# Optimization experiments

Measured on AMD Instinct MI355X. Metric: run time of the kernel, lower is better.

## Reference

```python
import jax, jax.numpy as jnp
import numpy as np

N_NODES = 100000
N_EDGES = 400000
N_GRAPHS = 1000
DIM = 5
N_OUT = 2
EPS = 1e-5


def _linear_params(key, fan_in, fan_out):
    kw, kb = jax.random.split(key)
    s = 1.0 / np.sqrt(fan_in)
    w = jax.random.uniform(kw, (fan_in, fan_out), minval=-s, maxval=s, dtype=jnp.float32)
    b = jax.random.uniform(kb, (fan_out,), minval=-s, maxval=s, dtype=jnp.float32)
    return w, b


def _gn_params(c):
    # rows: [weight, bias, mean_scale] as in PyG GraphNorm init (1, 0, 1)
    return jnp.stack([jnp.ones((c,)), jnp.zeros((c,)), jnp.ones((c,))], axis=0).astype(jnp.float32)


def setup_inputs() -> dict:
    key = jax.random.key(0)
    ks = jax.random.split(key, 16)
    x = jax.random.normal(ks[0], (N_NODES, DIM), dtype=jnp.float32)
    edge_index = jax.random.randint(ks[1], (2, N_EDGES), 0, N_NODES, dtype=jnp.int64)
    batch = jnp.sort(jax.random.randint(ks[2], (N_NODES,), 0, N_GRAPHS, dtype=jnp.int64))
    c1_w1, c1_b1 = _linear_params(ks[3], 2 * DIM, 128)
    c1_w2, c1_b2 = _linear_params(ks[4], 128, 128)
    c1_w3, c1_b3 = _linear_params(ks[5], 128, 128)
    c2_w1, c2_b1 = _linear_params(ks[6], 2 * 128, 256)
    c2_w2, c2_b2 = _linear_params(ks[7], 256, 256)
    c3_w1, c3_b1 = _linear_params(ks[8], 2 * 256, 256)
    lin_w1, lin_b1 = _linear_params(ks[9], 256, 256)
    lin_w2, lin_b2 = _linear_params(ks[10], 256, N_OUT)
    return {
        "x": x, "edge_index": edge_index, "batch": batch,
        "c1_w1": c1_w1, "c1_b1": c1_b1, "c1_gn1": _gn_params(128),
        "c1_w2": c1_w2, "c1_b2": c1_b2, "c1_gn2": _gn_params(128),
        "c1_w3": c1_w3, "c1_b3": c1_b3, "c1_gn3": _gn_params(128),
        "c2_w1": c2_w1, "c2_b1": c2_b1, "c2_gn1": _gn_params(256),
        "c2_w2": c2_w2, "c2_b2": c2_b2, "c2_gn2": _gn_params(256),
        "c3_w1": c3_w1, "c3_b1": c3_b1, "c3_gn1": _gn_params(256),
        "lin_w1": lin_w1, "lin_b1": lin_b1, "lin_w2": lin_w2, "lin_b2": lin_b2,
    }


def _graph_norm(h, p):
    # PyG GraphNorm with batch=None: normalize over all rows (single graph)
    g, b, ms = p[0], p[1], p[2]
    m = h.mean(axis=0)
    out = h - ms * m
    var = (out * out).mean(axis=0)
    return g * out * jax.lax.rsqrt(var + EPS) + b


def _edge_conv(x, src, dst, layers):
    # EdgeConv message: nn(cat[x_i, x_j - x_i]) aggregated (mean) at target i
    xi = x[dst]                                     # [E, C]
    h = jnp.concatenate([xi, x[src] - xi], axis=-1)  # [E, 2C]
    for w, b, gp in layers:
        h = jax.nn.relu(_graph_norm(h @ w + b, gp))
    s = jax.ops.segment_sum(h, dst, num_segments=N_NODES)
    ones = jnp.ones((dst.shape[0], 1), dtype=h.dtype)
    cnt = jax.ops.segment_sum(ones, dst, num_segments=N_NODES)
    return s / jnp.maximum(cnt, 1.0)


def reference(x, edge_index, batch,
              c1_w1, c1_b1, c1_gn1, c1_w2, c1_b2, c1_gn2, c1_w3, c1_b3, c1_gn3,
              c2_w1, c2_b1, c2_gn1, c2_w2, c2_b2, c2_gn2,
              c3_w1, c3_b1, c3_gn1,
              lin_w1, lin_b1, lin_w2, lin_b2):
    src, dst = edge_index[0], edge_index[1]
    h = _edge_conv(x, src, dst, [(c1_w1, c1_b1, c1_gn1), (c1_w2, c1_b2, c1_gn2), (c1_w3, c1_b3, c1_gn3)])
    h = _edge_conv(h, src, dst, [(c2_w1, c2_b1, c2_gn1), (c2_w2, c2_b2, c2_gn2)])
    h = _edge_conv(h, src, dst, [(c3_w1, c3_b1, c3_gn1)])
    # global_mean_pool over graphs (dropout = identity in eval)
    gs = jax.ops.segment_sum(h, batch, num_segments=N_GRAPHS)
    gc = jax.ops.segment_sum(jnp.ones((h.shape[0], 1), h.dtype), batch, num_segments=N_GRAPHS)
    g = gs / jnp.maximum(gc, 1.0)                   # [G, 256]
    out = jax.nn.relu(g @ lin_w1 + lin_b1) @ lin_w2 + lin_b2  # [G, n_out]
    return out
```

## Files before the change

kernel.cpp:

```cpp
#include <hip/hip_runtime.h>
#include <hip/hip_bf16.h>

#define NN 100000
#define NE 400000
#define NG 1000

typedef __attribute__((ext_vector_type(8))) short bf16x8;
typedef __attribute__((ext_vector_type(4))) float f32x4;

__device__ __forceinline__ float bf2f(unsigned short h) {
    return __uint_as_float((unsigned)h << 16);
}
__device__ __forceinline__ unsigned short f2bf(float f) {
    unsigned u = __float_as_uint(f);
    return (unsigned short)((u + 0x7FFFu + ((u >> 16) & 1u)) >> 16);
}
__device__ __forceinline__ void up8(uint4 u, float v[8]) {
    v[0] = bf2f((unsigned short)u.x); v[1] = bf2f((unsigned short)(u.x >> 16));
    v[2] = bf2f((unsigned short)u.y); v[3] = bf2f((unsigned short)(u.y >> 16));
    v[4] = bf2f((unsigned short)u.z); v[5] = bf2f((unsigned short)(u.z >> 16));
    v[6] = bf2f((unsigned short)u.w); v[7] = bf2f((unsigned short)(u.w >> 16));
}
__device__ __forceinline__ uint4 pk8(const float v[8]) {
    uint4 r;
    r.x = (uint)f2bf(v[0]) | ((uint)f2bf(v[1]) << 16);
    r.y = (uint)f2bf(v[2]) | ((uint)f2bf(v[3]) << 16);
    r.z = (uint)f2bf(v[4]) | ((uint)f2bf(v[5]) << 16);
    r.w = (uint)f2bf(v[6]) | ((uint)f2bf(v[7]) << 16);
    return r;
}

__global__ void diag_kernel(float* __restrict__ out, int n, float val) {
    int i = blockIdx.x * 256 + threadIdx.x;
    if (i < n) out[i] = val;
}

__global__ void deg_kernel(const int* __restrict__ dst, int* __restrict__ deg) {
    int e = blockIdx.x * 256 + threadIdx.x;
    if (e < NE) atomicAdd(&deg[dst[e]], 1);
}

__global__ void invdeg_kernel(const int* __restrict__ deg, float* __restrict__ invdeg) {
    int n = blockIdx.x * 256 + threadIdx.x;
    if (n < NN) invdeg[n] = 1.0f / (float)(deg[n] > 0 ? deg[n] : 1);
}

__global__ void conv1_node_kernel(const float* __restrict__ x, const float* __restrict__ W,
                                  unsigned short* __restrict__ RQ) {
    __shared__ float Ws[1280];
    for (int i = threadIdx.x; i < 1280; i += 256) Ws[i] = W[i];
    __syncthreads();
    int c = threadIdx.x & 127;
    int which = threadIdx.x >> 7;
    for (int n = blockIdx.x; n < NN; n += gridDim.x) {
        float acc = 0.f;
        #pragma unroll
        for (int r = 0; r < 5; r++) {
            float xv = x[n * 5 + r];
            float bot = Ws[(5 + r) * 128 + c];
            float w = which ? bot : (Ws[r * 128 + c] - bot);
            acc = fmaf(xv, w, acc);
        }
        RQ[(size_t)n * 256 + threadIdx.x] = f2bf(acc);
    }
}

__global__ void wtrans_kernel(const float* __restrict__ W, unsigned short* __restrict__ Wt,
                              int K, int N) {
    int idx = blockIdx.x * 256 + threadIdx.x;
    if (idx >= K * N) return;
    int c = idx / K, k = idx - c * K;
    Wt[(size_t)c * K + k] = f2bf(W[(size_t)k * N + c]);
}

__global__ void wprime_t_kernel(const float* __restrict__ W, unsigned short* __restrict__ Wpt,
                                int K, int C) {
    int idx = blockIdx.x * 256 + threadIdx.x;
    if (idx >= 2 * C * K) return;
    int n = idx / K, k = idx - n * K;
    float v;
    if (n < C) v = W[(size_t)k * C + n] - W[(size_t)(K + k) * C + n];
    else       v = W[(size_t)(K + k) * C + (n - C)];
    Wpt[(size_t)n * K + k] = f2bf(v);
}

template<int C>
__global__ void gstats_kernel(const unsigned short* __restrict__ RQ, const int* __restrict__ src,
                              const int* __restrict__ dst, const float* __restrict__ bias,
                              float* __restrict__ ssum, float* __restrict__ ssq) {
    constexpr int LPE = C / 8;
    constexpr int EPB = 256 / LPE;
    const int t = threadIdx.x;
    const int le = t % LPE, sub = t / LPE;
    const int c0 = le * 8;
    float4 b0 = *(const float4*)&bias[c0];
    float4 b1 = *(const float4*)&bias[c0 + 4];
    float bb[8] = {b0.x, b0.y, b0.z, b0.w, b1.x, b1.y, b1.z, b1.w};
    float ls[8], lq[8];
    #pragma unroll
    for (int i = 0; i < 8; i++) { ls[i] = 0.f; lq[i] = 0.f; }
    for (int e = blockIdx.x * EPB + sub; e < NE; e += gridDim.x * EPB) {
        int d = dst[e], s = src[e];
        uint4 rr = *(const uint4*)&RQ[(size_t)d * (2 * C) + c0];
        uint4 qq = *(const uint4*)&RQ[(size_t)s * (2 * C) + C + c0];
        float pr[8], pq[8];
        up8(rr, pr); up8(qq, pq);
        #pragma unroll
        for (int i = 0; i < 8; i++) {
            float v = pr[i] + pq[i] + bb[i];
            ls[i] += v; lq[i] += v * v;
        }
    }
    __shared__ float red[2][256][8];
    #pragma unroll
    for (int i = 0; i < 8; i++) { red[0][t][i] = ls[i]; red[1][t][i] = lq[i]; }
    __syncthreads();
    if (t < C) {
        int le2 = t >> 3, ch = t & 7;
        float s = 0.f, q = 0.f;
        #pragma unroll
        for (int g = 0; g < EPB; g++) {
            s += red[0][g * LPE + le2][ch];
            q += red[1][g * LPE + le2][ch];
        }
        atomicAdd(&ssum[t], s);
        atomicAdd(&ssq[t], q);
    }
}

__global__ void finalize_kernel(const float* __restrict__ ssum, const float* __restrict__ ssq,
                                const float* __restrict__ gn, int C, float invM,
                                float* __restrict__ alpha, float* __restrict__ beta) {
    int c = threadIdx.x;
    if (c >= C) return;
    float g = gn[c], b = gn[C + c], ms = gn[2 * C + c];
    float m = ssum[c] * invM;
    float var = ssq[c] * invM - m * m * ms * (2.f - ms);
    float inv = rsqrtf(var + 1e-5f);
    alpha[c] = g * inv;
    beta[c] = b - g * inv * ms * m;
}

template<int BN, bool GATHER, bool NORMRELU, bool ROWSC, bool STATS, bool STORE, bool SCAT,
         bool AF32>
__global__ __launch_bounds__(256) void mgemm_kernel(
    const void* __restrict__ Av, const int* __restrict__ gsrc, const int* __restrict__ gdst,
    const float* __restrict__ biasIn, const unsigned short* __restrict__ Wt,
    const float* __restrict__ alpha, const float* __restrict__ beta,
    const float* __restrict__ rowscale, const float* __restrict__ biasOut,
    unsigned short* __restrict__ Cmat, int M, int K, int N,
    float* __restrict__ ssum, float* __restrict__ ssq,
    const float* __restrict__ alphaO, const float* __restrict__ betaO,
    float* __restrict__ hsum) {
    constexpr int WNC = BN / 4;
    constexpr int NF = WNC / 16;
    __shared__ __align__(16) unsigned short At[2][64][40];
    __shared__ __align__(16) float sAl[256], sBe[256], sBi[256];
    __shared__ float sS[BN], sQ[BN];
    const int t = threadIdx.x;
    const int wave = t >> 6, lane = t & 63;
    const int l15 = lane & 15, lq = lane >> 4;
    const int r0 = blockIdx.y * 64;
    const int n0 = blockIdx.x * BN;
    const int srow = t >> 2, skq = t & 3;

    if (NORMRELU) for (int i = t; i < K; i += 256) { sAl[i] = alpha[i]; sBe[i] = beta[i]; }
    if (GATHER)   for (int i = t; i < K; i += 256) { sBi[i] = biasIn[i]; }
    if (STATS && t < BN) { sS[t] = 0.f; sQ[t] = 0.f; }

    const int ar = r0 + srow;
    int gd = 0, gs = 0;
    if (GATHER) { gd = gdst[ar]; gs = gsrc[ar]; }
    float rs = 1.f;
    if (ROWSC) rs = (ar < M) ? rowscale[ar] : 0.f;

    const unsigned short* Abf = (const unsigned short*)Av;
    const float* Af = (const float*)Av;

    const unsigned short* bp[NF];
    #pragma unroll
    for (int cf = 0; cf < NF; cf++)
        bp[cf] = &Wt[(size_t)(n0 + wave * WNC + 16 * cf + l15) * K + lq * 8];

    f32x4 acc[4][NF];
    #pragma unroll
    for (int i = 0; i < 4; i++)
        #pragma unroll
        for (int j = 0; j < NF; j++) acc[i][j] = {0.f, 0.f, 0.f, 0.f};

    uint4 rA, rQ;
    float4 fA0, fA1;
    auto loadRaw = [&](int k0, uint4& a, uint4& q, float4& f0, float4& f1) {
        int kb = k0 + skq * 8;
        if (GATHER) {
            a = *(const uint4*)&Abf[(size_t)gd * (2 * K) + kb];
            q = *(const uint4*)&Abf[(size_t)gs * (2 * K) + K + kb];
        } else if (AF32) {
            if (ar < M) {
                f0 = *(const float4*)&Af[(size_t)ar * K + kb];
                f1 = *(const float4*)&Af[(size_t)ar * K + kb + 4];
            } else { f0 = make_float4(0, 0, 0, 0); f1 = f0; }
        } else {
            if (ar < M) a = *(const uint4*)&Abf[(size_t)ar * K + kb];
            else a = make_uint4(0, 0, 0, 0);
        }
    };
    auto stage = [&](int k0, int buf, uint4 a, uint4 q, float4 f0, float4 f1) {
        int kb = k0 + skq * 8;
        float v[8];
        if (GATHER) {
            float pa[8], pq[8];
            up8(a, pa); up8(q, pq);
            float4 b0 = *(const float4*)&sBi[kb];
            float4 b1 = *(const float4*)&sBi[kb + 4];
            float bb[8] = {b0.x, b0.y, b0.z, b0.w, b1.x, b1.y, b1.z, b1.w};
            #pragma unroll
            for (int i = 0; i < 8; i++) v[i] = pa[i] + pq[i] + bb[i];
        } else if (AF32) {
            v[0] = f0.x; v[1] = f0.y; v[2] = f0.z; v[3] = f0.w;
            v[4] = f1.x; v[5] = f1.y; v[6] = f1.z; v[7] = f1.w;
        } else {
            up8(a, v);
        }
        if (NORMRELU) {
            float4 a0 = *(const float4*)&sAl[kb];
            float4 a1 = *(const float4*)&sAl[kb + 4];
            float4 e0 = *(const float4*)&sBe[kb];
            float4 e1 = *(const float4*)&sBe[kb + 4];
            float al[8] = {a0.x, a0.y, a0.z, a0.w, a1.x, a1.y, a1.z, a1.w};
            float be[8] = {e0.x, e0.y, e0.z, e0.w, e1.x, e1.y, e1.z, e1.w};
            #pragma unroll
            for (int i = 0; i < 8; i++) v[i] = fmaxf(fmaf(al[i], v[i], be[i]), 0.f);
        }
        if (ROWSC) {
            #pragma unroll
            for (int i = 0; i < 8; i++) v[i] *= rs;
        }
        *(uint4*)&At[buf][srow][skq * 8] = pk8(v);
    };

    loadRaw(0, rA, rQ, fA0, fA1);
    bf16x8 bcur[NF];
    #pragma unroll
    for (int cf = 0; cf < NF; cf++) bcur[cf] = *(const bf16x8*)(bp[cf] + 0);
    __syncthreads();
    stage(0, 0, rA, rQ, fA0, fA1);
    __syncthreads();

    int buf = 0;
    for (int k0 = 0; k0 < K; k0 += 32) {
        int nxt = k0 + 32;
        uint4 nA, nQ;
        float4 nf0, nf1;
        bf16x8 bnxt[NF];
        if (nxt < K) {
            loadRaw(nxt, nA, nQ, nf0, nf1);
            #pragma unroll
            for (int cf = 0; cf < NF; cf++) bnxt[cf] = *(const bf16x8*)(bp[cf] + nxt);
        }
        bf16x8 af[4];
        #pragma unroll
        for (int rf = 0; rf < 4; rf++)
            af[rf] = *(const bf16x8*)&At[buf][16 * rf + l15][lq * 8];
        #pragma unroll
        for (int rf = 0; rf < 4; rf++)
            #pragma unroll
            for (int cf = 0; cf < NF; cf++)
                acc[rf][cf] = __builtin_amdgcn_mfma_f32_16x16x32_bf16(
                    af[rf], bcur[cf], acc[rf][cf], 0, 0, 0);
        if (nxt < K) {
            stage(nxt, buf ^ 1, nA, nQ, nf0, nf1);
            __syncthreads();
            buf ^= 1;
            #pragma unroll
            for (int cf = 0; cf < NF; cf++) bcur[cf] = bnxt[cf];
        }
    }

    int cA[NF];
    float bO[NF], aO[NF], bOo[NF];
    #pragma unroll
    for (int cf = 0; cf < NF; cf++) {
        cA[cf] = n0 + wave * WNC + 16 * cf + l15;
        bO[cf] = (biasOut != nullptr) ? biasOut[cA[cf]] : 0.f;
        if (SCAT) { aO[cf] = alphaO[cA[cf]]; bOo[cf] = betaO[cA[cf]]; }
    }
    float ps[NF], pq[NF];
    #pragma unroll
    for (int cf = 0; cf < NF; cf++) { ps[cf] = 0.f; pq[cf] = 0.f; }
    #pragma unroll
    for (int rf = 0; rf < 4; rf++) {
        int rb = r0 + 16 * rf + lq * 4;
        int dd[4];
        if (SCAT) {
            #pragma unroll
            for (int jj = 0; jj < 4; jj++) dd[jj] = gdst[rb + jj];
        }
        #pragma unroll
        for (int cf = 0; cf < NF; cf++) {
            #pragma unroll
            for (int jj = 0; jj < 4; jj++) {
                float o = acc[rf][cf][jj] + bO[cf];
                if (STATS) { ps[cf] += o; pq[cf] += o * o; }
                if (STORE) {
                    int r = rb + jj;
                    if (r < M) Cmat[(size_t)r * N + cA[cf]] = f2bf(o);
                }
                if (SCAT) {
                    float h = fmaxf(fmaf(aO[cf], o, bOo[cf]), 0.f);
                    atomicAdd(&hsum[(size_t)dd[jj] * N + cA[cf]], h);
                }
            }
        }
    }
    if (STATS) {
        #pragma unroll
        for (int cf = 0; cf < NF; cf++) {
            float s = ps[cf], q = pq[cf];
            s += __shfl_xor(s, 16); s += __shfl_xor(s, 32);
            q += __shfl_xor(q, 16); q += __shfl_xor(q, 32);
            if (lq == 0) {
                atomicAdd(&sS[cA[cf] - n0], s);
                atomicAdd(&sQ[cA[cf] - n0], q);
            }
        }
        __syncthreads();
        if (t < BN) {
            atomicAdd(&ssum[n0 + t], sS[t]);
            atomicAdd(&ssq[n0 + t], sQ[t]);
        }
    }
}

template<int C>
__global__ void aggregate_kernel(const unsigned short* __restrict__ Y, const int* __restrict__ dst,
                                 const float* __restrict__ alpha, const float* __restrict__ beta,
                                 float* __restrict__ hsum) {
    constexpr int EPB = 256 / C;
    int c = threadIdx.x % C;
    int sub = threadIdx.x / C;
    float al = alpha[c], be = beta[c];
    for (int e = blockIdx.x * EPB + sub; e < NE; e += gridDim.x * EPB) {
        float v = fmaxf(fmaf(al, bf2f(Y[(size_t)e * C + c]), be), 0.f);
        atomicAdd(&hsum[(size_t)dst[e] * C + c], v);
    }
}

__global__ void aggregate_fg_kernel(const unsigned short* __restrict__ RQ,
                                    const int* __restrict__ src, const int* __restrict__ dst,
                                    const float* __restrict__ bias, const float* __restrict__ alpha,
                                    const float* __restrict__ beta, float* __restrict__ hsum) {
    int c = threadIdx.x;
    float b = bias[c], al = alpha[c], be = beta[c];
    for (int e = blockIdx.x; e < NE; e += gridDim.x) {
        int d = dst[e], s = src[e];
        float v = (bf2f(RQ[(size_t)d * 512 + c]) + bf2f(RQ[(size_t)s * 512 + 256 + c])) + b;
        float h = fmaxf(fmaf(al, v, be), 0.f);
        atomicAdd(&hsum[(size_t)d * 256 + c], h);
    }
}

__global__ void pool_kernel(const float* __restrict__ h3sum, const float* __restrict__ invdeg,
                            const int* __restrict__ batch, float* __restrict__ gsum,
                            int* __restrict__ gcnt) {
    int chunk = (NN + gridDim.x - 1) / gridDim.x;
    int nbeg = blockIdx.x * chunk;
    int nend = min(nbeg + chunk, NN);
    if (nbeg >= nend) return;
    int t = threadIdx.x;
    int curg = batch[nbeg];
    float acc = 0.f;
    int cnt = 0;
    for (int n = nbeg; n < nend; n++) {
        int g = batch[n];
        if (g != curg) {
            atomicAdd(&gsum[(size_t)curg * 256 + t], acc);
            if (t == 0) atomicAdd(&gcnt[curg], cnt);
            curg = g; acc = 0.f; cnt = 0;
        }
        acc += h3sum[(size_t)n * 256 + t] * invdeg[n];
        cnt++;
    }
    atomicAdd(&gsum[(size_t)curg * 256 + t], acc);
    if (t == 0) atomicAdd(&gcnt[curg], cnt);
}

__global__ void mlp_kernel(const float* __restrict__ gsum, const int* __restrict__ gcnt,
                           const float* __restrict__ W1, const float* __restrict__ b1,
                           const float* __restrict__ W2, const float* __restrict__ b2,
                           float* __restrict__ out) {
    int g = blockIdx.x;
    int t = threadIdx.x;
    __shared__ float grow[256];
    __shared__ float r0s[256], r1s[256];
    int cnt = gcnt[g];
    float inv = 1.0f / (float)(cnt > 0 ? cnt : 1);
    grow[t] = gsum[(size_t)g * 256 + t] * inv;
    __syncthreads();
    float acc = b1[t];
    for (int k = 0; k < 256; k++) acc = fmaf(grow[k], W1[k * 256 + t], acc);
    float h = fmaxf(acc, 0.f);
    r0s[t] = h * W2[t * 2 + 0];
    r1s[t] = h * W2[t * 2 + 1];
    __syncthreads();
    for (int s = 128; s > 0; s >>= 1) {
        if (t < s) { r0s[t] += r0s[t + s]; r1s[t] += r1s[t + s]; }
        __syncthreads();
    }
    if (t == 0) {
        out[g * 2 + 0] = r0s[0] + b2[0];
        out[g * 2 + 1] = r1s[0] + b2[1];
    }
}

extern "C" void kernel_launch(void* const* d_in, const int* in_sizes, int n_in,
                              void* d_out, int out_size, void* d_ws, size_t ws_size,
                              hipStream_t stream) {
    const float* x      = (const float*)d_in[0];
    const int*   ei     = (const int*)d_in[1];
    const int*   src    = ei;
    const int*   dstp   = ei + NE;
    const int*   batch  = (const int*)d_in[2];
    const float* c1_w1  = (const float*)d_in[3];
    const float* c1_b1  = (const float*)d_in[4];
    const float* c1_gn1 = (const float*)d_in[5];
    const float* c1_w2  = (const float*)d_in[6];
    const float* c1_b2  = (const float*)d_in[7];
    const float* c1_gn2 = (const float*)d_in[8];
    const float* c1_w3  = (const float*)d_in[9];
    const float* c1_b3  = (const float*)d_in[10];
    const float* c1_gn3 = (const float*)d_in[11];
    const float* c2_w1  = (const float*)d_in[12];
    const float* c2_b1  = (const float*)d_in[13];
    const float* c2_gn1 = (const float*)d_in[14];
    const float* c2_w2  = (const float*)d_in[15];
    const float* c2_b2  = (const float*)d_in[16];
    const float* c2_gn2 = (const float*)d_in[17];
    const float* c3_w1  = (const float*)d_in[18];
    const float* c3_b1  = (const float*)d_in[19];
    const float* c3_gn1 = (const float*)d_in[20];
    const float* lin_w1 = (const float*)d_in[21];
    const float* lin_b1 = (const float*)d_in[22];
    const float* lin_w2 = (const float*)d_in[23];
    const float* lin_b2 = (const float*)d_in[24];
    float* out = (float*)d_out;

    constexpr size_t REG_BYTES = (size_t)NE * 128 * 2;
    constexpr size_t NEED = 2 * REG_BYTES + 4 * 1024 * 1024;

    if (ws_size < NEED) {
        diag_kernel<<<(out_size + 255) / 256, 256, 0, stream>>>(
            out, out_size, (float)(ws_size >> 20));
        return;
    }

    char* base = (char*)d_ws;
    unsigned short* RA = (unsigned short*)base;
    unsigned short* RB = (unsigned short*)(base + REG_BYTES);
    float* h1sum = (float*)RB;
    float* h2sum = (float*)RB;
    float* h3sum = (float*)RB;
    char* p = base + 2 * REG_BYTES;
    auto alloc = [&](size_t bytes) -> void* {
        void* r = (void*)p;
        p += (bytes + 255) & ~(size_t)255;
        return r;
    };
    unsigned short* c1w2t = (unsigned short*)alloc((size_t)128 * 128 * 2);
    unsigned short* c1w3t = (unsigned short*)alloc((size_t)128 * 128 * 2);
    unsigned short* c2w2t = (unsigned short*)alloc((size_t)256 * 256 * 2);
    unsigned short* Wpt   = (unsigned short*)alloc((size_t)512 * 256 * 2);
    int*   deg    = (int*)alloc((size_t)NN * 4);
    float* invdeg = (float*)alloc((size_t)NN * 4);
    float* ssum   = (float*)alloc(256 * 4);
    float* ssq    = (float*)alloc(256 * 4);
    float* al0    = (float*)alloc(256 * 4);
    float* be0    = (float*)alloc(256 * 4);
    float* al1    = (float*)alloc(256 * 4);
    float* be1    = (float*)alloc(256 * 4);
    float* gsum   = (float*)alloc((size_t)NG * 256 * 4);
    int*   gcnt   = (int*)alloc((size_t)NG * 4);

    const float invE = 1.0f / (float)NE;
    const int MT_E = NE / 64;
    const int MT_N = (NN + 63) / 64;

    hipMemsetAsync(deg, 0, (size_t)NN * 4, stream);
    hipMemsetAsync(gsum, 0, (size_t)NG * 256 * 4, stream);
    hipMemsetAsync(gcnt, 0, (size_t)NG * 4, stream);

    deg_kernel<<<(NE + 255) / 256, 256, 0, stream>>>(dstp, deg);
    invdeg_kernel<<<(NN + 255) / 256, 256, 0, stream>>>(deg, invdeg);

    wtrans_kernel<<<(128 * 128 + 255) / 256, 256, 0, stream>>>(c1_w2, c1w2t, 128, 128);
    wtrans_kernel<<<(128 * 128 + 255) / 256, 256, 0, stream>>>(c1_w3, c1w3t, 128, 128);
    wtrans_kernel<<<(256 * 256 + 255) / 256, 256, 0, stream>>>(c2_w2, c2w2t, 256, 256);

    conv1_node_kernel<<<2048, 256, 0, stream>>>(x, c1_w1, RA);
    hipMemsetAsync(ssum, 0, 256 * 4, stream);
    hipMemsetAsync(ssq, 0, 256 * 4, stream);
    gstats_kernel<128><<<2048, 256, 0, stream>>>(RA, src, dstp, c1_b1, ssum, ssq);
    finalize_kernel<<<1, 256, 0, stream>>>(ssum, ssq, c1_gn1, 128, invE, al0, be0);

    hipMemsetAsync(ssum, 0, 256 * 4, stream);
    hipMemsetAsync(ssq, 0, 256 * 4, stream);
    mgemm_kernel<128, true, true, false, true, true, false, false>
        <<<dim3(1, MT_E), 256, 0, stream>>>(RA, src, dstp, c1_b1, c1w2t, al0, be0,
                                            nullptr, c1_b2, RB, NE, 128, 128,
                                            ssum, ssq, nullptr, nullptr, nullptr);
    finalize_kernel<<<1, 256, 0, stream>>>(ssum, ssq, c1_gn2, 128, invE, al0, be0);

    hipMemsetAsync(ssum, 0, 256 * 4, stream);
    hipMemsetAsync(ssq, 0, 256 * 4, stream);
    mgemm_kernel<128, false, true, false, true, true, false, false>
        <<<dim3(1, MT_E), 256, 0, stream>>>(RB, nullptr, nullptr, nullptr, c1w3t, al0, be0,
                                            nullptr, c1_b3, RA, NE, 128, 128,
                                            ssum, ssq, nullptr, nullptr, nullptr);
    finalize_kernel<<<1, 256, 0, stream>>>(ssum, ssq, c1_gn3, 128, invE, al0, be0);

    hipMemsetAsync(h1sum, 0, (size_t)NN * 128 * 4, stream);
    aggregate_kernel<128><<<2048, 256, 0, stream>>>(RA, dstp, al0, be0, h1sum);

    wprime_t_kernel<<<(512 * 128 + 255) / 256, 256, 0, stream>>>(c2_w1, Wpt, 128, 256);
    mgemm_kernel<256, false, false, true, false, true, false, true>
        <<<dim3(2, MT_N), 256, 0, stream>>>(h1sum, nullptr, nullptr, nullptr, Wpt,
                                            nullptr, nullptr, invdeg, nullptr, RA,
                                            NN, 128, 512, nullptr, nullptr,
                                            nullptr, nullptr, nullptr);
    hipMemsetAsync(ssum, 0, 256 * 4, stream);
    hipMemsetAsync(ssq, 0, 256 * 4, stream);
    gstats_kernel<256><<<2048, 256, 0, stream>>>(RA, src, dstp, c2_b1, ssum, ssq);
    finalize_kernel<<<1, 256, 0, stream>>>(ssum, ssq, c2_gn1, 256, invE, al0, be0);

    hipMemsetAsync(ssum, 0, 256 * 4, stream);
    hipMemsetAsync(ssq, 0, 256 * 4, stream);
    mgemm_kernel<256, true, true, false, true, false, false, false>
        <<<dim3(1, MT_E), 256, 0, stream>>>(RA, src, dstp, c2_b1, c2w2t, al0, be0,
                                            nullptr, c2_b2, nullptr, NE, 256, 256,
                                            ssum, ssq, nullptr, nullptr, nullptr);
    finalize_kernel<<<1, 256, 0, stream>>>(ssum, ssq, c2_gn2, 256, invE, al1, be1);

    hipMemsetAsync(h2sum, 0, (size_t)NN * 256 * 4, stream);
    mgemm_kernel<256, true, true, false, false, false, true, false>
        <<<dim3(1, MT_E), 256, 0, stream>>>(RA, src, dstp, c2_b1, c2w2t, al0, be0,
                                            nullptr, c2_b2, nullptr, NE, 256, 256,
                                            nullptr, nullptr, al1, be1, h2sum);

    wprime_t_kernel<<<(512 * 256 + 255) / 256, 256, 0, stream>>>(c3_w1, Wpt, 256, 256);
    mgemm_kernel<256, false, false, true, false, true, false, true>
        <<<dim3(2, MT_N), 256, 0, stream>>>(h2sum, nullptr, nullptr, nullptr, Wpt,
                                            nullptr, nullptr, invdeg, nullptr, RA,
                                            NN, 256, 512, nullptr, nullptr,
                                            nullptr, nullptr, nullptr);
    hipMemsetAsync(ssum, 0, 256 * 4, stream);
    hipMemsetAsync(ssq, 0, 256 * 4, stream);
    gstats_kernel<256><<<2048, 256, 0, stream>>>(RA, src, dstp, c3_b1, ssum, ssq);
    finalize_kernel<<<1, 256, 0, stream>>>(ssum, ssq, c3_gn1, 256, invE, al0, be0);

    hipMemsetAsync(h3sum, 0, (size_t)NN * 256 * 4, stream);
    aggregate_fg_kernel<<<2048, 256, 0, stream>>>(RA, src, dstp, c3_b1, al0, be0, h3sum);

    pool_kernel<<<512, 256, 0, stream>>>(h3sum, invdeg, batch, gsum, gcnt);
    mlp_kernel<<<NG, 256, 0, stream>>>(gsum, gcnt, lin_w1, lin_b1, lin_w2, lin_b2, out);
}
```

Measured before the change: 2.286 ms.

## Stage full-K A tile in LDS once instead of double-buffered K loop

The GEMM kernel now takes K as a compile-time template parameter and loads the entire 64xK A tile, with gather, norm and relu applied, into shared memory in one pass before the MFMA loop. The old version used a double-buffered 32-wide K pipeline with a barrier each step. Removing the per-step barriers and issuing all gather loads up front is meant to expose more memory-level parallelism, and the K loop is now fully unrolled. In exchange, LDS use grows (up to 64x264 bf16 for K=256), which may lower occupancy. B-operand loads are also no longer prefetched ahead of the MFMAs.

```diff
diff --git a/kernel.cpp b/kernel.cpp
--- a/kernel.cpp
+++ b/kernel.cpp
@@ -141,140 +141,113 @@
     beta[c] = b - g * inv * ms * m;
 }
 
-template<int BN, bool GATHER, bool NORMRELU, bool ROWSC, bool STATS, bool STORE, bool SCAT,
-         bool AF32>
+template<int TK, int BN, bool GATHER, bool NORMRELU, bool ROWSC, bool STATS, bool STORE,
+         bool SCAT, bool AF32>
 __global__ __launch_bounds__(256) void mgemm_kernel(
     const void* __restrict__ Av, const int* __restrict__ gsrc, const int* __restrict__ gdst,
     const float* __restrict__ biasIn, const unsigned short* __restrict__ Wt,
     const float* __restrict__ alpha, const float* __restrict__ beta,
     const float* __restrict__ rowscale, const float* __restrict__ biasOut,
-    unsigned short* __restrict__ Cmat, int M, int K, int N,
+    unsigned short* __restrict__ Cmat, int M, int N,
     float* __restrict__ ssum, float* __restrict__ ssq,
     const float* __restrict__ alphaO, const float* __restrict__ betaO,
     float* __restrict__ hsum) {
     constexpr int WNC = BN / 4;
     constexpr int NF = WNC / 16;
-    __shared__ __align__(16) unsigned short At[2][64][40];
-    __shared__ __align__(16) float sAl[256], sBe[256], sBi[256];
+    constexpr int SPR = TK / 8;
+    constexpr int ITER = 64 * SPR / 256;
+    __shared__ __align__(16) unsigned short At[64][TK + 8];
+    __shared__ __align__(16) float sAl[TK], sBe[TK], sBi[TK];
     __shared__ float sS[BN], sQ[BN];
     const int t = threadIdx.x;
     const int wave = t >> 6, lane = t & 63;
     const int l15 = lane & 15, lq = lane >> 4;
     const int r0 = blockIdx.y * 64;
     const int n0 = blockIdx.x * BN;
-    const int srow = t >> 2, skq = t & 3;
-
-    if (NORMRELU) for (int i = t; i < K; i += 256) { sAl[i] = alpha[i]; sBe[i] = beta[i]; }
-    if (GATHER)   for (int i = t; i < K; i += 256) { sBi[i] = biasIn[i]; }
+
+    if (NORMRELU) for (int i = t; i < TK; i += 256) { sAl[i] = alpha[i]; sBe[i] = beta[i]; }
+    if (GATHER)   for (int i = t; i < TK; i += 256) { sBi[i] = biasIn[i]; }
     if (STATS && t < BN) { sS[t] = 0.f; sQ[t] = 0.f; }
-
-    const int ar = r0 + srow;
-    int gd = 0, gs = 0;
-    if (GATHER) { gd = gdst[ar]; gs = gsrc[ar]; }
-    float rs = 1.f;
-    if (ROWSC) rs = (ar < M) ? rowscale[ar] : 0.f;
+    __syncthreads();
 
     const unsigned short* Abf = (const unsigned short*)Av;
     const float* Af = (const float*)Av;
 
-    const unsigned short* bp[NF];
-    #pragma unroll
-    for (int cf = 0; cf < NF; cf++)
-        bp[cf] = &Wt[(size_t)(n0 + wave * WNC + 16 * cf + l15) * K + lq * 8];
-
-    f32x4 acc[4][NF];
-    #pragma unroll
-    for (int i = 0; i < 4; i++)
-        #pragma unroll
-        for (int j = 0; j < NF; j++) acc[i][j] = {0.f, 0.f, 0.f, 0.f};
-
-    uint4 rA, rQ;
-    float4 fA0, fA1;
-    auto loadRaw = [&](int k0, uint4& a, uint4& q, float4& f0, float4& f1) {
-        int kb = k0 + skq * 8;
+    #pragma unroll
+    for (int it = 0; it < ITER; it++) {
+        int slot = it * 256 + t;
+        int row = slot / SPR;
+        int c0 = (slot - row * SPR) * 8;
+        int ar = r0 + row;
+        float v[8];
         if (GATHER) {
-            a = *(const uint4*)&Abf[(size_t)gd * (2 * K) + kb];
-            q = *(const uint4*)&Abf[(size_t)gs * (2 * K) + K + kb];
+            int gd = gdst[ar], gs = gsrc[ar];
+            uint4 pa4 = *(const uint4*)&Abf[(size_t)gd * (2 * TK) + c0];
+            uint4 pq4 = *(const uint4*)&Abf[(size_t)gs * (2 * TK) + TK + c0];
+            float pa[8], pq[8];
+            up8(pa4, pa); up8(pq4, pq);
+            #pragma unroll
+            for (int i = 0; i < 8; i++) v[i] = pa[i] + pq[i] + sBi[c0 + i];
         } else if (AF32) {
             if (ar < M) {
-                f0 = *(const float4*)&Af[(size_t)ar * K + kb];
-                f1 = *(const float4*)&Af[(size_t)ar * K + kb + 4];
-            } else { f0 = make_float4(0, 0, 0, 0); f1 = f0; }
+                float4 f0 = *(const float4*)&Af[(size_t)ar * TK + c0];
+                float4 f1 = *(const float4*)&Af[(size_t)ar * TK + c0 + 4];
+                v[0] = f0.x; v[1] = f0.y; v[2] = f0.z; v[3] = f0.w;
+                v[4] = f1.x; v[5] = f1.y; v[6] = f1.z; v[7] = f1.w;
+            } else {
+                #pragma unroll
+                for (int i = 0; i < 8; i++) v[i] = 0.f;
+            }
         } else {
-            if (ar < M) a = *(const uint4*)&Abf[(size_t)ar * K + kb];
-            else a = make_uint4(0, 0, 0, 0);
-        }
-    };
-    auto stage = [&](int k0, int buf, uint4 a, uint4 q, float4 f0, float4 f1) {
-        int kb = k0 + skq * 8;
-        float v[8];
-        if (GATHER) {
-            float pa[8], pq[8];
-            up8(a, pa); up8(q, pq);
-            float4 b0 = *(const float4*)&sBi[kb];
-            float4 b1 = *(const float4*)&sBi[kb + 4];
-            float bb[8] = {b0.x, b0.y, b0.z, b0.w, b1.x, b1.y, b1.z, b1.w};
+            if (ar < M) {
+                uint4 a4 = *(const uint4*)&Abf[(size_t)ar * TK + c0];
+                up8(a4, v);
+            } else {
+                #pragma unroll
+                for (int i = 0; i < 8; i++) v[i] = 0.f;
+            }
+        }
+        if (NORMRELU) {
             #pragma unroll
-            for (int i = 0; i < 8; i++) v[i] = pa[i] + pq[i] + bb[i];
-        } else if (AF32) {
-            v[0] = f0.x; v[1] = f0.y; v[2] = f0.z; v[3] = f0.w;
-            v[4] = f1.x; v[5] = f1.y; v[6] = f1.z; v[7] = f1.w;
-        } else {
-            up8(a, v);
-        }
-        if (NORMRELU) {
-            float4 a0 = *(const float4*)&sAl[kb];
-            float4 a1 = *(const float4*)&sAl[kb + 4];
-            float4 e0 = *(const float4*)&sBe[kb];
-            float4 e1 = *(const float4*)&sBe[kb + 4];
-            float al[8] = {a0.x, a0.y, a0.z, a0.w, a1.x, a1.y, a1.z, a1.w};
-            float be[8] = {e0.x, e0.y, e0.z, e0.w, e1.x, e1.y, e1.z, e1.w};
-            #pragma unroll
-            for (int i = 0; i < 8; i++) v[i] = fmaxf(fmaf(al[i], v[i], be[i]), 0.f);
+            for (int i = 0; i < 8; i++)
+                v[i] = fmaxf(fmaf(sAl[c0 + i], v[i], sBe[c0 + i]), 0.f);
         }
         if (ROWSC) {
+            float rs = (ar < M) ? rowscale[ar] : 0.f;
             #pragma unroll
             for (int i = 0; i < 8; i++) v[i] *= rs;
         }
-        *(uint4*)&At[buf][srow][skq * 8] = pk8(v);
-    };
-
-    loadRaw(0, rA, rQ, fA0, fA1);
-    bf16x8 bcur[NF];
-    #pragma unroll
-    for (int cf = 0; cf < NF; cf++) bcur[cf] = *(const bf16x8*)(bp[cf] + 0);
+        *(uint4*)&At[row][c0] = pk8(v);
+    }
     __syncthreads();
-    stage(0, 0, rA, rQ, fA0, fA1);
-    __syncthreads();
-
-    int buf = 0;
-    for (int k0 = 0; k0 < K; k0 += 32) {
-        int nxt = k0 + 32;
-        uint4 nA, nQ;
-        float4 nf0, nf1;
-        bf16x8 bnxt[NF];
-        if (nxt < K) {
-            loadRaw(nxt, nA, nQ, nf0, nf1);
-            #pragma unroll
-            for (int cf = 0; cf < NF; cf++) bnxt[cf] = *(const bf16x8*)(bp[cf] + nxt);
-        }
+
+    const unsigned short* bp[NF];
+    #pragma unroll
+    for (int cf = 0; cf < NF; cf++)
+        bp[cf] = &Wt[(size_t)(n0 + wave * WNC + 16 * cf + l15) * TK + lq * 8];
+
+    f32x4 acc[4][NF];
+    #pragma unroll
+    for (int i = 0; i < 4; i++)
+        #pragma unroll
+        for (int j = 0; j < NF; j++) acc[i][j] = {0.f, 0.f, 0.f, 0.f};
+
+    #pragma unroll
+    for (int k0 = 0; k0 < TK; k0 += 32) {
         bf16x8 af[4];
         #pragma unroll
         for (int rf = 0; rf < 4; rf++)
-            af[rf] = *(const bf16x8*)&At[buf][16 * rf + l15][lq * 8];
+            af[rf] = *(const bf16x8*)&At[16 * rf + l15][k0 + lq * 8];
+        bf16x8 bfr[NF];
+        #pragma unroll
+        for (int cf = 0; cf < NF; cf++)
+            bfr[cf] = *(const bf16x8*)(bp[cf] + k0);
         #pragma unroll
         for (int rf = 0; rf < 4; rf++)
             #pragma unroll
             for (int cf = 0; cf < NF; cf++)
                 acc[rf][cf] = __builtin_amdgcn_mfma_f32_16x16x32_bf16(
-                    af[rf], bcur[cf], acc[rf][cf], 0, 0, 0);
-        if (nxt < K) {
-            stage(nxt, buf ^ 1, nA, nQ, nf0, nf1);
-            __syncthreads();
-            buf ^= 1;
-            #pragma unroll
-            for (int cf = 0; cf < NF; cf++) bcur[cf] = bnxt[cf];
-        }
+                    af[rf], bfr[cf], acc[rf][cf], 0, 0, 0);
     }
 
     int cA[NF];
@@ -504,17 +477,17 @@
 
     hipMemsetAsync(ssum, 0, 256 * 4, stream);
     hipMemsetAsync(ssq, 0, 256 * 4, stream);
-    mgemm_kernel<128, true, true, false, true, true, false, false>
+    mgemm_kernel<128, 128, true, true, false, true, true, false, false>
         <<<dim3(1, MT_E), 256, 0, stream>>>(RA, src, dstp, c1_b1, c1w2t, al0, be0,
-                                            nullptr, c1_b2, RB, NE, 128, 128,
+                                            nullptr, c1_b2, RB, NE, 128,
                                             ssum, ssq, nullptr, nullptr, nullptr);
     finalize_kernel<<<1, 256, 0, stream>>>(ssum, ssq, c1_gn2, 128, invE, al0, be0);
 
     hipMemsetAsync(ssum, 0, 256 * 4, stream);
     hipMemsetAsync(ssq, 0, 256 * 4, stream);
-    mgemm_kernel<128, false, true, false, true, true, false, false>
+    mgemm_kernel<128, 128, false, true, false, true, true, false, false>
         <<<dim3(1, MT_E), 256, 0, stream>>>(RB, nullptr, nullptr, nullptr, c1w3t, al0, be0,
-                                            nullptr, c1_b3, RA, NE, 128, 128,
+                                            nullptr, c1_b3, RA, NE, 128,
                                             ssum, ssq, nullptr, nullptr, nullptr);
     finalize_kernel<<<1, 256, 0, stream>>>(ssum, ssq, c1_gn3, 128, invE, al0, be0);
 
@@ -522,10 +495,10 @@
     aggregate_kernel<128><<<2048, 256, 0, stream>>>(RA, dstp, al0, be0, h1sum);
 
     wprime_t_kernel<<<(512 * 128 + 255) / 256, 256, 0, stream>>>(c2_w1, Wpt, 128, 256);
-    mgemm_kernel<256, false, false, true, false, true, false, true>
+    mgemm_kernel<128, 256, false, false, true, false, true, false, true>
         <<<dim3(2, MT_N), 256, 0, stream>>>(h1sum, nullptr, nullptr, nullptr, Wpt,
                                             nullptr, nullptr, invdeg, nullptr, RA,
-                                            NN, 128, 512, nullptr, nullptr,
+                                            NN, 512, nullptr, nullptr,
                                             nullptr, nullptr, nullptr);
     hipMemsetAsync(ssum, 0, 256 * 4, stream);
     hipMemsetAsync(ssq, 0, 256 * 4, stream);
@@ -534,23 +507,23 @@
 
     hipMemsetAsync(ssum, 0, 256 * 4, stream);
     hipMemsetAsync(ssq, 0, 256 * 4, stream);
-    mgemm_kernel<256, true, true, false, true, false, false, false>
+    mgemm_kernel<256, 256, true, true, false, true, false, false, false>
         <<<dim3(1, MT_E), 256, 0, stream>>>(RA, src, dstp, c2_b1, c2w2t, al0, be0,
-                                            nullptr, c2_b2, nullptr, NE, 256, 256,
+                                            nullptr, c2_b2, nullptr, NE, 256,
                                             ssum, ssq, nullptr, nullptr, nullptr);
     finalize_kernel<<<1, 256, 0, stream>>>(ssum, ssq, c2_gn2, 256, invE, al1, be1);
 
     hipMemsetAsync(h2sum, 0, (size_t)NN * 256 * 4, stream);
-    mgemm_kernel<256, true, true, false, false, false, true, false>
+    mgemm_kernel<256, 256, true, true, false, false, false, true, false>
         <<<dim3(1, MT_E), 256, 0, stream>>>(RA, src, dstp, c2_b1, c2w2t, al0, be0,
-                                            nullptr, c2_b2, nullptr, NE, 256, 256,
+                                            nullptr, c2_b2, nullptr, NE, 256,
                                             nullptr, nullptr, al1, be1, h2sum);
 
     wprime_t_kernel<<<(512 * 256 + 255) / 256, 256, 0, stream>>>(c3_w1, Wpt, 256, 256);
-    mgemm_kernel<256, false, false, true, false, true, false, true>
+    mgemm_kernel<256, 256, false, false, true, false, true, false, true>
         <<<dim3(2, MT_N), 256, 0, stream>>>(h2sum, nullptr, nullptr, nullptr, Wpt,
                                             nullptr, nullptr, invdeg, nullptr, RA,
-                                            NN, 256, 512, nullptr, nullptr,
+                                            NN, 512, nullptr, nullptr,
                                             nullptr, nullptr, nullptr);
     hipMemsetAsync(ssum, 0, 256 * 4, stream);
     hipMemsetAsync(ssq, 0, 256 * 4, stream);
```

After: 2.209 ms. 3.3% less time.
